# Performance work log

Measured on AMD Instinct MI355X. Metric: run time of the kernel, lower is better.

## Reference

```python
import jax, jax.numpy as jnp
import numpy as np

N, E, D, L = 50000, 600000, 128, 3
EPS = 1e-5


def _layer_norm(x, g, b):
    m = jnp.mean(x, axis=-1, keepdims=True)
    v = jnp.mean((x - m) ** 2, axis=-1, keepdims=True)
    return (x - m) * jax.lax.rsqrt(v + EPS) * g + b


def setup_inputs() -> dict:
    key = jax.random.key(0)
    ks = jax.random.split(key, 20)
    s = 1.0 / np.sqrt(D)
    inp = {
        "node": jax.random.normal(ks[0], (N, D), jnp.float32),
        "edge_attr": jax.random.uniform(ks[1], (E,), jnp.float32),
        # stacked per-layer parameters [L, ...]
        "W_rel": jax.random.uniform(ks[2], (L, D, D), jnp.float32, -s, s),
        "b_rel": jax.random.uniform(ks[3], (L, D), jnp.float32, -s, s),
        "W_root": jax.random.uniform(ks[4], (L, D, D), jnp.float32, -s, s),
        "ln1_g": jnp.ones((L, D), jnp.float32),
        "ln1_b": jnp.zeros((L, D), jnp.float32),
        "ln2_g": jnp.ones((L, D), jnp.float32),
        "ln2_b": jnp.zeros((L, D), jnp.float32),
        "W1": jax.random.uniform(ks[5], (L, D, D), jnp.float32, -s, s),
        "b1": jax.random.uniform(ks[6], (L, D), jnp.float32, -s, s),
        "W2": jax.random.uniform(ks[7], (L, D, D), jnp.float32, -s, s),
        "b2": jax.random.uniform(ks[8], (L, D), jnp.float32, -s, s),
        "jk_W": jax.random.uniform(ks[9], (L * D, D), jnp.float32, -1.0 / np.sqrt(L * D), 1.0 / np.sqrt(L * D)),
        "jk_b": jax.random.uniform(ks[10], (D,), jnp.float32, -1.0 / np.sqrt(L * D), 1.0 / np.sqrt(L * D)),
        "edge_index": jax.random.randint(ks[11], (2, E), 0, N, jnp.int64),
        "batch_ptr": jnp.sort(jax.random.randint(ks[12], (51,), 0, N, jnp.int64)),
    }
    return inp


def reference(node, edge_attr, W_rel, b_rel, W_root, ln1_g, ln1_b, ln2_g, ln2_b,
              W1, b1, W2, b2, jk_W, jk_b, edge_index, batch_ptr):
    src, dst = edge_index[0], edge_index[1]
    deg = jax.ops.segment_sum(jnp.ones((E,), node.dtype), dst, num_segments=N)
    inv_deg = 1.0 / jnp.maximum(deg, 1.0)  # nodes with no in-edges -> 0 aggregate
    outs = []
    for l in range(L):
        msg = node[src] * edge_attr[:, None]                       # [E, D] gather
        agg = jax.ops.segment_sum(msg, dst, num_segments=N)        # scatter-sum
        mean = agg * inv_deg[:, None]                              # mean aggregation
        # GraphConv: lin_rel(aggr) + lin_root(x); skip_connection=False
        node = mean @ W_rel[l] + b_rel[l] + node @ W_root[l]
        node = jax.nn.relu(_layer_norm(node @ W1[l] + b1[l], ln1_g[l], ln1_b[l]))
        node = jax.nn.relu(_layer_norm(node @ W2[l] + b2[l], ln2_g[l], ln2_b[l]))
        outs.append(node)
    jk = jnp.concatenate(outs, axis=-1)                            # [N, L*D]
    return jk @ jk_W + jk_b
```

## Files before the change

kernel.cpp:

```cpp
#include <hip/hip_runtime.h>

#define NN 50000
#define EE 600000
#define DD 128
#define CAP 64
#define CNTSTRIDE 16
#define LDS_STRIDE 136

typedef __attribute__((ext_vector_type(8))) short bf16x8;
typedef __attribute__((ext_vector_type(4))) float f32x4;

__device__ __forceinline__ unsigned short f2bf(float f) {
    union { float f; unsigned u; } v; v.f = f;
    unsigned r = v.u + 0x7FFF + ((v.u >> 16) & 1);
    return (unsigned short)(r >> 16);
}
__device__ __forceinline__ float bflo(unsigned x) { return __uint_as_float(x << 16); }
__device__ __forceinline__ float bfhi(unsigned x) { return __uint_as_float(x & 0xffff0000u); }

#define FILL_BLKS  2344
#define CONV_BLKS  6250
__global__ void setup_kernel(const int* __restrict__ src, const int* __restrict__ dst,
                             const float* __restrict__ ea,
                             int* __restrict__ cnt, unsigned* __restrict__ slots,
                             const float* __restrict__ nodef, unsigned short* __restrict__ node_bf,
                             const float* __restrict__ W_rel, const float* __restrict__ W_root,
                             const float* __restrict__ W1, float* __restrict__ Wc,
                             const float* __restrict__ b_rel, const float* __restrict__ b1,
                             float* __restrict__ bc) {
    int b = blockIdx.x;
    if (b < FILL_BLKS) {
        int e = b * 256 + threadIdx.x;
        if (e >= EE) return;
        int d = dst[e];
        int p = atomicAdd(&cnt[d * CNTSTRIDE], 1);
        if (p < CAP) {
            unsigned w16 = (unsigned)__float2int_rn(ea[e] * 65535.0f);
            if (w16 > 65535u) w16 = 65535u;
            slots[d * CAP + p] = ((unsigned)src[e] << 16) | w16;
        }
    } else if (b < FILL_BLKS + CONV_BLKS) {
        int i = (b - FILL_BLKS) * 256 + threadIdx.x;
        float4 v = *(const float4*)&nodef[(size_t)i * 4];
        ushort4 o;
        o.x = f2bf(v.x); o.y = f2bf(v.y); o.z = f2bf(v.z); o.w = f2bf(v.w);
        *(ushort4*)&node_bf[(size_t)i * 4] = o;
    } else if (b < FILL_BLKS + CONV_BLKS + 96) {
        int bb = b - FILL_BLKS - CONV_BLKS;
        int which = bb >> 4, part = bb & 15;
        int l = (which < 3) ? which : which - 3;
        const float* A = (which < 3) ? (W_rel + (size_t)l * 16384) : (W_root + (size_t)l * 16384);
        const float* B = W1 + (size_t)l * 16384;
        float* out = Wc + (size_t)which * 16384;
        int o = part * 1024 + threadIdx.x;
        for (int rep = 0; rep < 4; ++rep, o += 256) {
            int i = o >> 7, j = o & 127;
            float s = 0.f;
            for (int k = 0; k < 128; ++k) s = fmaf(A[i * 128 + k], B[k * 128 + j], s);
            out[o] = s;
        }
    } else {
        int l = b - FILL_BLKS - CONV_BLKS - 96;
        int j = threadIdx.x;
        if (j < 128) {
            float s = 0.f;
            for (int k = 0; k < 128; ++k)
                s = fmaf(b_rel[l * 128 + k], W1[(size_t)l * 16384 + k * 128 + j], s);
            bc[l * 128 + j] = s + b1[l * 128 + j];
        }
    }
}

__global__ void pack_w_kernel(const float* __restrict__ Wc, const float* __restrict__ W2,
                              const float* __restrict__ jkW, unsigned short* __restrict__ packed) {
    int t = blockIdx.x * 256 + threadIdx.x;
    int chunk = t >> 11;
    int r = t & 2047;
    int lane = r & 63;
    int tile = r >> 6;
    int kt = tile >> 3, nt = tile & 7;
    int quad = lane >> 4, n = lane & 15;
    const float* src;
    if (chunk < 6)       src = Wc  + (size_t)chunk * 16384;
    else if (chunk < 9)  src = W2  + (size_t)(chunk - 6) * 16384;
    else                 src = jkW + (size_t)(chunk - 9) * 16384;
    int k0 = kt * 32 + quad * 8;
    int col = nt * 16 + n;
    union { unsigned short u[8]; uint4 v; } tmp;
#pragma unroll
    for (int j = 0; j < 8; ++j) tmp.u[j] = f2bf(src[(size_t)(k0 + j) * DD + col]);
    *(uint4*)&packed[(size_t)t * 8] = tmp.v;
}

__global__ __launch_bounds__(256) void gather_mean_kernel(
    const unsigned short* __restrict__ feat,
    const unsigned* __restrict__ slots,
    const int* __restrict__ cnt,
    unsigned short* __restrict__ mean) {
    const int node = (int)((blockIdx.x * 256 + threadIdx.x) >> 6);
    if (node >= NN) return;
    const int lane = threadIdx.x & 63;
    const int g  = lane >> 4;
    const int h8 = (lane & 15) * 8;
    int c = cnt[node * CNTSTRIDE];
    if (c > CAP) c = CAP;
    const unsigned* sp = slots + (size_t)node * CAP;

    float acc[8] = {0.f, 0.f, 0.f, 0.f, 0.f, 0.f, 0.f, 0.f};
    const float wscale = 1.0f / 65535.0f;

    for (int j0 = 0; j0 < c; j0 += 16) {
        uint4 sv = *(const uint4*)&sp[j0 + g * 4];
        unsigned se[4] = {sv.x, sv.y, sv.z, sv.w};
#pragma unroll
        for (int t = 0; t < 4; ++t) {
            int idx = j0 + g * 4 + t;
            bool ok = idx < c;
            unsigned e = se[t];
            int   srcn = ok ? (int)(e >> 16) : 0;
            float w    = ok ? (float)(e & 0xffffu) * wscale : 0.0f;
            uint4 v = *(const uint4*)&feat[(size_t)srcn * DD + h8];
            acc[0] = fmaf(bflo(v.x), w, acc[0]);
            acc[1] = fmaf(bfhi(v.x), w, acc[1]);
            acc[2] = fmaf(bflo(v.y), w, acc[2]);
            acc[3] = fmaf(bfhi(v.y), w, acc[3]);
            acc[4] = fmaf(bflo(v.z), w, acc[4]);
            acc[5] = fmaf(bfhi(v.z), w, acc[5]);
            acc[6] = fmaf(bflo(v.w), w, acc[6]);
            acc[7] = fmaf(bfhi(v.w), w, acc[7]);
        }
    }

#pragma unroll
    for (int k = 0; k < 8; ++k) {
        acc[k] += __shfl_xor(acc[k], 16);
        acc[k] += __shfl_xor(acc[k], 32);
    }

    if (g == 0) {
        float id = 1.0f / fmaxf((float)c, 1.0f);
        union { unsigned short u[8]; uint4 v; } o;
#pragma unroll
        for (int k = 0; k < 8; ++k) o.u[k] = f2bf(acc[k] * id);
        *(uint4*)&mean[(size_t)node * DD + h8] = o.v;
    }
}

template <bool JK>
__global__ __launch_bounds__(256) void fused_layer(
    const unsigned short* __restrict__ mean, const unsigned short* __restrict__ nodef,
    const unsigned short* __restrict__ PWrel, const unsigned short* __restrict__ PWroot,
    const unsigned short* __restrict__ PW2,
    const float* __restrict__ bc, const float* __restrict__ ln1g, const float* __restrict__ ln1b,
    const float* __restrict__ b2, const float* __restrict__ ln2g, const float* __restrict__ ln2b,
    unsigned short* __restrict__ out,
    const unsigned short* __restrict__ o0, const unsigned short* __restrict__ o1,
    const unsigned short* __restrict__ PJ0, const unsigned short* __restrict__ PJ1,
    const unsigned short* __restrict__ PJ2,
    const float* __restrict__ jkb, float* __restrict__ fout) {
    __shared__ unsigned short relay[4][16 * LDS_STRIDE];
    const int lane = threadIdx.x & 63;
    const int wid  = threadIdx.x >> 6;
    const int mrow = blockIdx.x * 64 + wid * 16;
    if (mrow >= NN) return;

    const int quad = lane >> 4, n15 = lane & 15;
    const int kq   = quad * 8;
    unsigned short* wt = relay[wid];

    const unsigned short* Am = mean  + (size_t)(mrow + n15) * DD;
    const unsigned short* An = nodef + (size_t)(mrow + n15) * DD;

    f32x4 acc[8];
#pragma unroll
    for (int nt = 0; nt < 8; ++nt) acc[nt] = (f32x4){0.f, 0.f, 0.f, 0.f};
#pragma unroll
    for (int kt = 0; kt < 4; ++kt) {
        bf16x8 am = *(const bf16x8*)&Am[kt * 32 + kq];
        bf16x8 an = *(const bf16x8*)&An[kt * 32 + kq];
#pragma unroll
        for (int nt = 0; nt < 8; ++nt) {
            bf16x8 brel = *(const bf16x8*)&PWrel[(size_t)((kt * 8 + nt) * 64 + lane) * 8];
            acc[nt] = __builtin_amdgcn_mfma_f32_16x16x32_bf16(am, brel, acc[nt], 0, 0, 0);
            bf16x8 brt = *(const bf16x8*)&PWroot[(size_t)((kt * 8 + nt) * 64 + lane) * 8];
            acc[nt] = __builtin_amdgcn_mfma_f32_16x16x32_bf16(an, brt, acc[nt], 0, 0, 0);
        }
    }

    float x[8][4];
#pragma unroll
    for (int nt = 0; nt < 8; ++nt) {
        float bv = bc[nt * 16 + n15];
#pragma unroll
        for (int r = 0; r < 4; ++r) x[nt][r] = acc[nt][r] + bv;
    }
    {
        float s[4] = {0, 0, 0, 0}, q[4] = {0, 0, 0, 0};
#pragma unroll
        for (int nt = 0; nt < 8; ++nt)
#pragma unroll
            for (int r = 0; r < 4; ++r) { s[r] += x[nt][r]; q[r] += x[nt][r] * x[nt][r]; }
#pragma unroll
        for (int m = 1; m <= 8; m <<= 1)
#pragma unroll
            for (int r = 0; r < 4; ++r) { s[r] += __shfl_xor(s[r], m); q[r] += __shfl_xor(q[r], m); }
        const float inv = 1.0f / 128.0f;
#pragma unroll
        for (int r = 0; r < 4; ++r) {
            float mu = s[r] * inv;
            float rs = rsqrtf(fmaxf(q[r] * inv - mu * mu, 0.0f) + 1e-5f);
#pragma unroll
            for (int nt = 0; nt < 8; ++nt) {
                float g = ln1g[nt * 16 + n15], bb = ln1b[nt * 16 + n15];
                x[nt][r] = fmaxf((x[nt][r] - mu) * rs * g + bb, 0.0f);
            }
        }
    }

#pragma unroll
    for (int nt = 0; nt < 8; ++nt)
#pragma unroll
        for (int r = 0; r < 4; ++r)
            wt[(quad * 4 + r) * LDS_STRIDE + nt * 16 + n15] = f2bf(x[nt][r]);
    __asm__ __volatile__("s_waitcnt lgkmcnt(0)" ::: "memory");

    f32x4 acc2[8];
#pragma unroll
    for (int nt = 0; nt < 8; ++nt) acc2[nt] = (f32x4){0.f, 0.f, 0.f, 0.f};
#pragma unroll
    for (int kt = 0; kt < 4; ++kt) {
        bf16x8 ah = *(const bf16x8*)&wt[n15 * LDS_STRIDE + kt * 32 + kq];
#pragma unroll
        for (int nt = 0; nt < 8; ++nt) {
            bf16x8 bw = *(const bf16x8*)&PW2[(size_t)((kt * 8 + nt) * 64 + lane) * 8];
            acc2[nt] = __builtin_amdgcn_mfma_f32_16x16x32_bf16(ah, bw, acc2[nt], 0, 0, 0);
        }
    }
#pragma unroll
    for (int nt = 0; nt < 8; ++nt) {
        float bv = b2[nt * 16 + n15];
#pragma unroll
        for (int r = 0; r < 4; ++r) x[nt][r] = acc2[nt][r] + bv;
    }
    {
        float s[4] = {0, 0, 0, 0}, q[4] = {0, 0, 0, 0};
#pragma unroll
        for (int nt = 0; nt < 8; ++nt)
#pragma unroll
            for (int r = 0; r < 4; ++r) { s[r] += x[nt][r]; q[r] += x[nt][r] * x[nt][r]; }
#pragma unroll
        for (int m = 1; m <= 8; m <<= 1)
#pragma unroll
            for (int r = 0; r < 4; ++r) { s[r] += __shfl_xor(s[r], m); q[r] += __shfl_xor(q[r], m); }
        const float inv = 1.0f / 128.0f;
#pragma unroll
        for (int r = 0; r < 4; ++r) {
            float mu = s[r] * inv;
            float rs = rsqrtf(fmaxf(q[r] * inv - mu * mu, 0.0f) + 1e-5f);
#pragma unroll
            for (int nt = 0; nt < 8; ++nt) {
                float g = ln2g[nt * 16 + n15], bb = ln2b[nt * 16 + n15];
                x[nt][r] = fmaxf((x[nt][r] - mu) * rs * g + bb, 0.0f);
            }
        }
    }

    __asm__ __volatile__("s_waitcnt lgkmcnt(0)" ::: "memory");
#pragma unroll
    for (int nt = 0; nt < 8; ++nt)
#pragma unroll
        for (int r = 0; r < 4; ++r)
            wt[(quad * 4 + r) * LDS_STRIDE + nt * 16 + n15] = f2bf(x[nt][r]);
    __asm__ __volatile__("s_waitcnt lgkmcnt(0)" ::: "memory");

    if constexpr (!JK) {
#pragma unroll
        for (int i = 0; i < 4; ++i) {
            int s = i * 512 + lane * 8;
            int r = s >> 7, col = s & 127;
            uint4 v = *(const uint4*)&wt[r * LDS_STRIDE + col];
            *(uint4*)&out[(size_t)(mrow + r) * DD + col] = v;
        }
    } else {
        f32x4 accJ[8];
#pragma unroll
        for (int nt = 0; nt < 8; ++nt) accJ[nt] = (f32x4){0.f, 0.f, 0.f, 0.f};
#pragma unroll
        for (int kt = 0; kt < 4; ++kt) {
            bf16x8 ah = *(const bf16x8*)&wt[n15 * LDS_STRIDE + kt * 32 + kq];
#pragma unroll
            for (int nt = 0; nt < 8; ++nt) {
                bf16x8 bw = *(const bf16x8*)&PJ2[(size_t)((kt * 8 + nt) * 64 + lane) * 8];
                accJ[nt] = __builtin_amdgcn_mfma_f32_16x16x32_bf16(ah, bw, accJ[nt], 0, 0, 0);
            }
        }
        const unsigned short* A0 = o0 + (size_t)(mrow + n15) * DD;
        const unsigned short* A1 = o1 + (size_t)(mrow + n15) * DD;
#pragma unroll
        for (int kt = 0; kt < 4; ++kt) {
            bf16x8 a0 = *(const bf16x8*)&A0[kt * 32 + kq];
            bf16x8 a1 = *(const bf16x8*)&A1[kt * 32 + kq];
#pragma unroll
            for (int nt = 0; nt < 8; ++nt) {
                bf16x8 b0 = *(const bf16x8*)&PJ0[(size_t)((kt * 8 + nt) * 64 + lane) * 8];
                accJ[nt] = __builtin_amdgcn_mfma_f32_16x16x32_bf16(a0, b0, accJ[nt], 0, 0, 0);
                bf16x8 b1 = *(const bf16x8*)&PJ1[(size_t)((kt * 8 + nt) * 64 + lane) * 8];
                accJ[nt] = __builtin_amdgcn_mfma_f32_16x16x32_bf16(a1, b1, accJ[nt], 0, 0, 0);
            }
        }
#pragma unroll
        for (int nt = 0; nt < 8; ++nt) {
            float bv = jkb[nt * 16 + n15];
#pragma unroll
            for (int r = 0; r < 4; ++r)
                fout[(size_t)(mrow + quad * 4 + r) * DD + nt * 16 + n15] = accJ[nt][r] + bv;
        }
    }
}

extern "C" void kernel_launch(void* const* d_in, const int* in_sizes, int n_in,
                              void* d_out, int out_size, void* d_ws, size_t ws_size,
                              hipStream_t stream) {
    const float* node   = (const float*)d_in[0];
    const float* ea     = (const float*)d_in[1];
    const float* W_rel  = (const float*)d_in[2];
    const float* b_rel  = (const float*)d_in[3];
    const float* W_root = (const float*)d_in[4];
    const float* ln1_g  = (const float*)d_in[5];
    const float* ln1_b  = (const float*)d_in[6];
    const float* ln2_g  = (const float*)d_in[7];
    const float* ln2_b  = (const float*)d_in[8];
    const float* W1     = (const float*)d_in[9];
    const float* b1     = (const float*)d_in[10];
    const float* W2     = (const float*)d_in[11];
    const float* b2     = (const float*)d_in[12];
    const float* jk_W   = (const float*)d_in[13];
    const float* jk_b   = (const float*)d_in[14];
    const int*   ei     = (const int*)d_in[15];
    const int* srcI = ei;
    const int* dstI = ei + EE;

    char* ws = (char*)d_ws;
    size_t off = 0;
    auto alloc = [&](size_t bytes) {
        void* p = ws + off;
        off += (bytes + 255) & ~(size_t)255;
        return p;
    };
    int*            cnt     = (int*)alloc((size_t)NN * CNTSTRIDE * 4);
    unsigned*       slots   = (unsigned*)alloc((size_t)NN * CAP * 4);
    unsigned short* node_bf = (unsigned short*)alloc((size_t)NN * DD * 2);
    unsigned short* mean_bf = (unsigned short*)alloc((size_t)NN * DD * 2);
    unsigned short* outs_bf[2];
    for (int l = 0; l < 2; ++l) outs_bf[l] = (unsigned short*)alloc((size_t)NN * DD * 2);
    float*          Wc      = (float*)alloc((size_t)6 * 16384 * 4);
    float*          bc      = (float*)alloc((size_t)3 * 128 * 4);
    unsigned short* packed  = (unsigned short*)alloc((size_t)12 * 16384 * 2);

    hipMemsetAsync(cnt, 0, (size_t)NN * CNTSTRIDE * 4, stream);
    setup_kernel<<<FILL_BLKS + CONV_BLKS + 96 + 3, 256, 0, stream>>>(
        srcI, dstI, ea, cnt, slots, node, node_bf, W_rel, W_root, W1, Wc, b_rel, b1, bc);
    pack_w_kernel<<<12 * 2048 / 256, 256, 0, stream>>>(Wc, W2, jk_W, packed);

    const int gblocks = (NN + 63) / 64;
    unsigned short* cur = node_bf;
    for (int l = 0; l < 3; ++l) {
        gather_mean_kernel<<<NN / 4, 256, 0, stream>>>(cur, slots, cnt, mean_bf);
        if (l < 2) {
            fused_layer<false><<<gblocks, 256, 0, stream>>>(
                mean_bf, cur,
                packed + (size_t)l * 16384, packed + (size_t)(3 + l) * 16384,
                packed + (size_t)(6 + l) * 16384,
                bc + (size_t)l * DD, ln1_g + (size_t)l * DD, ln1_b + (size_t)l * DD,
                b2 + (size_t)l * DD, ln2_g + (size_t)l * DD, ln2_b + (size_t)l * DD,
                outs_bf[l],
                nullptr, nullptr, nullptr, nullptr, nullptr, nullptr, nullptr);
            cur = outs_bf[l];
        } else {
            fused_layer<true><<<gblocks, 256, 0, stream>>>(
                mean_bf, cur,
                packed + (size_t)l * 16384, packed + (size_t)(3 + l) * 16384,
                packed + (size_t)(6 + l) * 16384,
                bc + (size_t)l * DD, ln1_g + (size_t)l * DD, ln1_b + (size_t)l * DD,
                b2 + (size_t)l * DD, ln2_g + (size_t)l * DD, ln2_b + (size_t)l * DD,
                nullptr,
                outs_bf[0], outs_bf[1],
                packed + (size_t)9 * 16384, packed + (size_t)10 * 16384, packed + (size_t)11 * 16384,
                jk_b, (float*)d_out);
        }
    }
}
```

Before: 302.3 us.

## Replace global-atomic CSR fill with two-pass binned sort through shared memory

Builds the per-node slot lists in two passes instead of global atomics per edge. The first pass bins edges by destination block of 256 nodes with a block-local histogram and scan in shared memory. The second pass assembles each 128-node half-bin's slot lists in LDS and writes them out as coalesced stores. It also merges the W_rel/W_root·W1 weight fold into the packing kernel, drops the intermediate Wc buffer and a launch, and shrinks the cnt array from strided to dense. The cost is an extra kernel, a staging buffer of records, and a fixed per-bin capacity that could overflow and silently drop edges on skewed graphs.

```diff
diff --git a/kernel.cpp b/kernel.cpp
--- a/kernel.cpp
+++ b/kernel.cpp
@@ -4,8 +4,13 @@
 #define EE 600000
 #define DD 128
 #define CAP 64
-#define CNTSTRIDE 16
+#define BINS 196
+#define NP (BINS * 256)
+#define BINCAP 3584
+#define BCSTRIDE 16
 #define LDS_STRIDE 136
+#define P1_EDGES 2048
+#define P1_BLOCKS ((EE + P1_EDGES - 1) / P1_EDGES)
 
 typedef __attribute__((ext_vector_type(8))) short bf16x8;
 typedef __attribute__((ext_vector_type(4))) float f32x4;
@@ -18,78 +23,159 @@
 __device__ __forceinline__ float bflo(unsigned x) { return __uint_as_float(x << 16); }
 __device__ __forceinline__ float bfhi(unsigned x) { return __uint_as_float(x & 0xffff0000u); }
 
-#define FILL_BLKS  2344
-#define CONV_BLKS  6250
-__global__ void setup_kernel(const int* __restrict__ src, const int* __restrict__ dst,
-                             const float* __restrict__ ea,
-                             int* __restrict__ cnt, unsigned* __restrict__ slots,
-                             const float* __restrict__ nodef, unsigned short* __restrict__ node_bf,
-                             const float* __restrict__ W_rel, const float* __restrict__ W_root,
-                             const float* __restrict__ W1, float* __restrict__ Wc,
-                             const float* __restrict__ b_rel, const float* __restrict__ b1,
-                             float* __restrict__ bc) {
+__global__ __launch_bounds__(256) void fill_p1(
+    const int* __restrict__ src, const int* __restrict__ dst, const float* __restrict__ ea,
+    int* __restrict__ binCnt, unsigned long long* __restrict__ recs) {
+    __shared__ int hist[BINS];
+    __shared__ int lstart[BINS];
+    __shared__ int gbase[BINS];
+    __shared__ int scan[256];
+    __shared__ unsigned long long srt[P1_EDGES];
+    const int t = threadIdx.x;
+    for (int i = t; i < BINS; i += 256) hist[i] = 0;
+    __syncthreads();
+
+    unsigned long long rec[8];
+    int bin[8], rnk[8];
+    bool val[8];
+#pragma unroll
+    for (int g = 0; g < 2; ++g) {
+        int e0 = blockIdx.x * P1_EDGES + g * 1024 + t * 4;
+        int4 dv, sv; float4 ev;
+        if (e0 + 3 < EE) {
+            dv = *(const int4*)&dst[e0];
+            sv = *(const int4*)&src[e0];
+            ev = *(const float4*)&ea[e0];
+        } else {
+            int* dp = (int*)&dv; int* sp = (int*)&sv; float* ep = (float*)&ev;
+#pragma unroll
+            for (int k = 0; k < 4; ++k) {
+                int e = e0 + k;
+                dp[k] = (e < EE) ? dst[e] : 0;
+                sp[k] = (e < EE) ? src[e] : 0;
+                ep[k] = (e < EE) ? ea[e] : 0.f;
+            }
+        }
+#pragma unroll
+        for (int k = 0; k < 4; ++k) {
+            int i = g * 4 + k;
+            int e = e0 + k;
+            val[i] = (e < EE);
+            int d = ((const int*)&dv)[k];
+            unsigned w16 = (unsigned)__float2int_rn(((const float*)&ev)[k] * 65535.0f);
+            if (w16 > 65535u) w16 = 65535u;
+            rec[i] = ((unsigned long long)(unsigned)d << 32) |
+                     (((unsigned)((const int*)&sv)[k]) << 16) | w16;
+            bin[i] = d >> 8;
+            rnk[i] = val[i] ? atomicAdd(&hist[bin[i]], 1) : 0;
+        }
+    }
+    __syncthreads();
+    scan[t] = (t < BINS) ? hist[t] : 0;
+    __syncthreads();
+#pragma unroll
+    for (int off = 1; off < 256; off <<= 1) {
+        int v = (t >= off) ? scan[t - off] : 0;
+        __syncthreads();
+        scan[t] += v;
+        __syncthreads();
+    }
+    if (t < BINS) {
+        lstart[t] = scan[t] - hist[t];
+        gbase[t] = hist[t] ? atomicAdd(&binCnt[t * BCSTRIDE], hist[t]) : 0;
+    }
+    __syncthreads();
+#pragma unroll
+    for (int i = 0; i < 8; ++i)
+        if (val[i]) srt[lstart[bin[i]] + rnk[i]] = rec[i];
+    __syncthreads();
+    const int total = scan[255];
+    for (int j = t; j < total; j += 256) {
+        unsigned long long r = srt[j];
+        int b = (int)(r >> 40);
+        int o = gbase[b] + (j - lstart[b]);
+        if (o < BINCAP) recs[(size_t)b * BINCAP + o] = r;
+    }
+}
+
+__global__ __launch_bounds__(256) void fill_p2(
+    const int* __restrict__ binCnt, const unsigned long long* __restrict__ recs,
+    int* __restrict__ cnt, unsigned* __restrict__ slots) {
+    __shared__ int cl[128];
+    __shared__ unsigned sl[128 * CAP];
+    const int b = blockIdx.x >> 1, half = blockIdx.x & 1, t = threadIdx.x;
+    if (t < 128) cl[t] = 0;
+    __syncthreads();
+    int n = binCnt[b * BCSTRIDE];
+    if (n > BINCAP) n = BINCAP;
+    const unsigned long long* rp = recs + (size_t)b * BINCAP;
+    for (int j = t; j < n; j += 256) {
+        unsigned long long r = rp[j];
+        int dl = (int)(r >> 32) & 255;
+        if ((dl >> 7) == half) {
+            int p = atomicAdd(&cl[dl & 127], 1);
+            if (p < CAP) sl[(dl & 127) * CAP + p] = (unsigned)r;
+        }
+    }
+    __syncthreads();
+    const int node0 = (b << 8) + (half << 7);
+    if (t < 128) cnt[node0 + t] = cl[t];
+    const uint4* s4 = (const uint4*)sl;
+    uint4* g4 = (uint4*)(slots + (size_t)node0 * CAP);
+    for (int i = t; i < 2048; i += 256) g4[i] = s4[i];
+}
+
+#define CONV_BLKS 6250
+__global__ void prep_kernel(const float* __restrict__ nodef, unsigned short* __restrict__ node_bf,
+                            const float* __restrict__ W_rel, const float* __restrict__ W_root,
+                            const float* __restrict__ W1, const float* __restrict__ W2,
+                            const float* __restrict__ jkW,
+                            const float* __restrict__ b_rel, const float* __restrict__ b1,
+                            float* __restrict__ bc, unsigned short* __restrict__ packed) {
     int b = blockIdx.x;
-    if (b < FILL_BLKS) {
-        int e = b * 256 + threadIdx.x;
-        if (e >= EE) return;
-        int d = dst[e];
-        int p = atomicAdd(&cnt[d * CNTSTRIDE], 1);
-        if (p < CAP) {
-            unsigned w16 = (unsigned)__float2int_rn(ea[e] * 65535.0f);
-            if (w16 > 65535u) w16 = 65535u;
-            slots[d * CAP + p] = ((unsigned)src[e] << 16) | w16;
-        }
-    } else if (b < FILL_BLKS + CONV_BLKS) {
-        int i = (b - FILL_BLKS) * 256 + threadIdx.x;
+    if (b < 96) {
+        int tg = b * 256 + threadIdx.x;
+        int chunk = tg >> 11, r = tg & 2047;
+        int lane = r & 63, tile = r >> 6;
+        int kt = tile >> 3, nt = tile & 7;
+        int quad = lane >> 4, n = lane & 15;
+        int k0 = kt * 32 + quad * 8;
+        int col = nt * 16 + n;
+        union { unsigned short u[8]; uint4 v; } tmp;
+        if (chunk < 6) {
+            int l = (chunk < 3) ? chunk : chunk - 3;
+            const float* A = ((chunk < 3) ? W_rel : W_root) + (size_t)l * 16384;
+            const float* B = W1 + (size_t)l * 16384;
+            float acc[8] = {0.f, 0.f, 0.f, 0.f, 0.f, 0.f, 0.f, 0.f};
+            for (int k = 0; k < 128; ++k) {
+                float bv = B[k * 128 + col];
+#pragma unroll
+                for (int j = 0; j < 8; ++j) acc[j] = fmaf(A[(k0 + j) * 128 + k], bv, acc[j]);
+            }
+#pragma unroll
+            for (int j = 0; j < 8; ++j) tmp.u[j] = f2bf(acc[j]);
+        } else {
+            const float* s = (chunk < 9) ? (W2 + (size_t)(chunk - 6) * 16384)
+                                         : (jkW + (size_t)(chunk - 9) * 16384);
+#pragma unroll
+            for (int j = 0; j < 8; ++j) tmp.u[j] = f2bf(s[(size_t)(k0 + j) * DD + col]);
+        }
+        *(uint4*)&packed[(size_t)tg * 8] = tmp.v;
+    } else if (b == 96) {
+        for (int o = threadIdx.x; o < 384; o += 256) {
+            int l = o >> 7, j = o & 127;
+            float s = 0.f;
+            for (int k = 0; k < 128; ++k)
+                s = fmaf(b_rel[l * 128 + k], W1[(size_t)l * 16384 + k * 128 + j], s);
+            bc[o] = s + b1[o];
+        }
+    } else {
+        int i = (b - 97) * 256 + threadIdx.x;
         float4 v = *(const float4*)&nodef[(size_t)i * 4];
         ushort4 o;
         o.x = f2bf(v.x); o.y = f2bf(v.y); o.z = f2bf(v.z); o.w = f2bf(v.w);
         *(ushort4*)&node_bf[(size_t)i * 4] = o;
-    } else if (b < FILL_BLKS + CONV_BLKS + 96) {
-        int bb = b - FILL_BLKS - CONV_BLKS;
-        int which = bb >> 4, part = bb & 15;
-        int l = (which < 3) ? which : which - 3;
-        const float* A = (which < 3) ? (W_rel + (size_t)l * 16384) : (W_root + (size_t)l * 16384);
-        const float* B = W1 + (size_t)l * 16384;
-        float* out = Wc + (size_t)which * 16384;
-        int o = part * 1024 + threadIdx.x;
-        for (int rep = 0; rep < 4; ++rep, o += 256) {
-            int i = o >> 7, j = o & 127;
-            float s = 0.f;
-            for (int k = 0; k < 128; ++k) s = fmaf(A[i * 128 + k], B[k * 128 + j], s);
-            out[o] = s;
-        }
-    } else {
-        int l = b - FILL_BLKS - CONV_BLKS - 96;
-        int j = threadIdx.x;
-        if (j < 128) {
-            float s = 0.f;
-            for (int k = 0; k < 128; ++k)
-                s = fmaf(b_rel[l * 128 + k], W1[(size_t)l * 16384 + k * 128 + j], s);
-            bc[l * 128 + j] = s + b1[l * 128 + j];
-        }
-    }
-}
-
-__global__ void pack_w_kernel(const float* __restrict__ Wc, const float* __restrict__ W2,
-                              const float* __restrict__ jkW, unsigned short* __restrict__ packed) {
-    int t = blockIdx.x * 256 + threadIdx.x;
-    int chunk = t >> 11;
-    int r = t & 2047;
-    int lane = r & 63;
-    int tile = r >> 6;
-    int kt = tile >> 3, nt = tile & 7;
-    int quad = lane >> 4, n = lane & 15;
-    const float* src;
-    if (chunk < 6)       src = Wc  + (size_t)chunk * 16384;
-    else if (chunk < 9)  src = W2  + (size_t)(chunk - 6) * 16384;
-    else                 src = jkW + (size_t)(chunk - 9) * 16384;
-    int k0 = kt * 32 + quad * 8;
-    int col = nt * 16 + n;
-    union { unsigned short u[8]; uint4 v; } tmp;
-#pragma unroll
-    for (int j = 0; j < 8; ++j) tmp.u[j] = f2bf(src[(size_t)(k0 + j) * DD + col]);
-    *(uint4*)&packed[(size_t)t * 8] = tmp.v;
+    }
 }
 
 __global__ __launch_bounds__(256) void gather_mean_kernel(
@@ -102,7 +188,7 @@
     const int lane = threadIdx.x & 63;
     const int g  = lane >> 4;
     const int h8 = (lane & 15) * 8;
-    int c = cnt[node * CNTSTRIDE];
+    int c = cnt[node];
     if (c > CAP) c = CAP;
     const unsigned* sp = slots + (size_t)node * CAP;
 
@@ -347,20 +433,22 @@
         off += (bytes + 255) & ~(size_t)255;
         return p;
     };
-    int*            cnt     = (int*)alloc((size_t)NN * CNTSTRIDE * 4);
-    unsigned*       slots   = (unsigned*)alloc((size_t)NN * CAP * 4);
-    unsigned short* node_bf = (unsigned short*)alloc((size_t)NN * DD * 2);
-    unsigned short* mean_bf = (unsigned short*)alloc((size_t)NN * DD * 2);
+    int*                binCnt  = (int*)alloc((size_t)BINS * BCSTRIDE * 4);
+    unsigned long long* recs    = (unsigned long long*)alloc((size_t)BINS * BINCAP * 8);
+    int*                cnt     = (int*)alloc((size_t)NP * 4);
+    unsigned*           slots   = (unsigned*)alloc((size_t)NP * CAP * 4);
+    unsigned short*     node_bf = (unsigned short*)alloc((size_t)NN * DD * 2);
+    unsigned short*     mean_bf = (unsigned short*)alloc((size_t)NN * DD * 2);
     unsigned short* outs_bf[2];
     for (int l = 0; l < 2; ++l) outs_bf[l] = (unsigned short*)alloc((size_t)NN * DD * 2);
-    float*          Wc      = (float*)alloc((size_t)6 * 16384 * 4);
-    float*          bc      = (float*)alloc((size_t)3 * 128 * 4);
-    unsigned short* packed  = (unsigned short*)alloc((size_t)12 * 16384 * 2);
-
-    hipMemsetAsync(cnt, 0, (size_t)NN * CNTSTRIDE * 4, stream);
-    setup_kernel<<<FILL_BLKS + CONV_BLKS + 96 + 3, 256, 0, stream>>>(
-        srcI, dstI, ea, cnt, slots, node, node_bf, W_rel, W_root, W1, Wc, b_rel, b1, bc);
-    pack_w_kernel<<<12 * 2048 / 256, 256, 0, stream>>>(Wc, W2, jk_W, packed);
+    float*              bc      = (float*)alloc((size_t)3 * 128 * 4);
+    unsigned short*     packed  = (unsigned short*)alloc((size_t)12 * 16384 * 2);
+
+    hipMemsetAsync(binCnt, 0, (size_t)BINS * BCSTRIDE * 4, stream);
+    fill_p1<<<P1_BLOCKS, 256, 0, stream>>>(srcI, dstI, ea, binCnt, recs);
+    fill_p2<<<BINS * 2, 256, 0, stream>>>(binCnt, recs, cnt, slots);
+    prep_kernel<<<97 + CONV_BLKS, 256, 0, stream>>>(
+        node, node_bf, W_rel, W_root, W1, W2, jk_W, b_rel, b1, bc, packed);
 
     const int gblocks = (NN + 63) / 64;
     unsigned short* cur = node_bf;
```

After: 290.5 us. 1.04x faster.
